# Kernel tuning notes

Measured on AMD Instinct MI355X. Metric: run time of the kernel, lower is better.

The kernel has to match this reference:

```python
import jax, jax.numpy as jnp
import numpy as np


def setup_inputs() -> dict:
    key = jax.random.key(0)
    k1, k2, k3 = jax.random.split(key, 3)
    N, K, H, W = 8, 8, 256, 256
    C, P = 32, 100000
    fragments = jax.random.randint(k1, (N, K, H, W), 0, P, dtype=jnp.int64)
    alphas = jax.random.uniform(k2, (N, K, H, W), dtype=jnp.float32)
    features = jax.random.normal(k3, (C, P), dtype=jnp.float32)
    return {"fragments": fragments, "alphas": alphas, "features": features}


def reference(fragments, alphas, features):
    # Alpha compositing (front-to-back over the K points-per-pixel axis):
    #   weight_k = alpha_k * prod_{j<k} (1 - alpha_j)
    #   out[n,c,h,w] = sum_k weight_k[n,k,h,w] * features[c, fragments[n,k,h,w]]
    # Indices < 0 mark empty fragment slots (sorted to the tail by the
    # rasterizer); treat them as alpha = 0 so they contribute nothing and
    # do not attenuate.
    valid = fragments >= 0                                   # (N,K,H,W)
    a = jnp.where(valid, alphas, 0.0)                        # (N,K,H,W)
    # exclusive cumulative product of transmittance (1 - alpha) along K
    trans = jnp.cumprod(1.0 - a, axis=1)                     # inclusive
    excl = jnp.concatenate(
        [jnp.ones_like(trans[:, :1]), trans[:, :-1]], axis=1
    )                                                        # exclusive
    weights = a * excl                                       # (N,K,H,W)
    idx = jnp.where(valid, fragments, 0)
    gathered = features[:, idx]                              # (C,N,K,H,W)
    images = jnp.einsum("cnkhw,nkhw->nchw", gathered, weights)
    return images
```

## Files before the change

kernel.cpp:

```cpp
#include <hip/hip_runtime.h>
#include <hip/hip_fp16.h>

#define N_IMG 8
#define K_LAY 8
#define C_CH  32
#define P_FEAT 100000
#define HW 65536
#define NPIX (N_IMG * HW)

#define T_EPS 3e-3f

__global__ __launch_bounds__(256) void transpose_feat_h(
    const float* __restrict__ feat, __half* __restrict__ featT)
{
    __shared__ float tile[32][33];
    const int x  = threadIdx.x;
    const int y  = threadIdx.y;
    const int p0 = blockIdx.x * 32;

    #pragma unroll
    for (int j = 0; j < 4; ++j) {
        const int c = y * 4 + j;
        tile[c][x] = feat[(size_t)c * P_FEAT + p0 + x];
    }
    __syncthreads();

    const int t  = x + 32 * y;
    const int pl = t >> 3;
    const int c0 = (t & 7) * 4;
    union { __half h[4]; unsigned long long u; } pk;
    #pragma unroll
    for (int j = 0; j < 4; ++j)
        pk.h[j] = __float2half(tile[c0 + j][pl]);
    *reinterpret_cast<unsigned long long*>(
        featT + (size_t)(p0 + pl) * C_CH + c0) = pk.u;
}

__global__ __launch_bounds__(256) void composite(
    const int*    __restrict__ frag,
    const float*  __restrict__ alpha,
    const __half* __restrict__ featT,
    float*        __restrict__ out)
{
    const int tid = blockIdx.x * 256 + threadIdx.x;
    const int pix = tid >> 2;
    const int q   = tid & 3;
    const int n   = pix >> 16;
    const int p   = pix & (HW - 1);

    const int*   fb = frag  + (size_t)n * K_LAY * HW + p;
    const float* ab = alpha + (size_t)n * K_LAY * HW + p;

    int   f[K_LAY];
    float a[K_LAY];
    #pragma unroll
    for (int k = 0; k < K_LAY; ++k) f[k] = fb[(size_t)k * HW];
    #pragma unroll
    for (int k = 0; k < K_LAY; ++k) a[k] = ab[(size_t)k * HW];

    float w[K_LAY];
    int   idx[K_LAY];
    float T = 1.0f;
    #pragma unroll
    for (int k = 0; k < K_LAY; ++k) {
        const bool  valid = (f[k] >= 0);
        const float ak    = valid ? a[k] : 0.0f;
        const bool  live  = (T >= T_EPS) && valid;
        w[k]   = live ? ak * T : 0.0f;
        idx[k] = live ? f[k] : 0;
        T *= (1.0f - ak);
    }

    float acc[8];
    #pragma unroll
    for (int c = 0; c < 8; ++c) acc[c] = 0.0f;

    #pragma unroll
    for (int k = 0; k < K_LAY; ++k) {
        const float4 r = *reinterpret_cast<const float4*>(
            featT + (size_t)idx[k] * C_CH + q * 8);
        const float wk = w[k];
        const __half2* hp = reinterpret_cast<const __half2*>(&r);
        #pragma unroll
        for (int j = 0; j < 4; ++j) {
            const float2 fj = __half22float2(hp[j]);
            acc[j*2 + 0] = fmaf(wk, fj.x, acc[j*2 + 0]);
            acc[j*2 + 1] = fmaf(wk, fj.y, acc[j*2 + 1]);
        }
    }

    float* ob = out + ((size_t)n * C_CH + q * 8) * HW + p;
    #pragma unroll
    for (int j = 0; j < 8; ++j)
        ob[(size_t)j * HW] = acc[j];
}

__global__ __launch_bounds__(256) void composite_strided(
    const int*   __restrict__ frag,
    const float* __restrict__ alpha,
    const float* __restrict__ feat,
    float*       __restrict__ out)
{
    const int gid = blockIdx.x * 256 + threadIdx.x;
    const int n = gid >> 16;
    const int p = gid & (HW - 1);

    const int*   fb = frag  + (size_t)n * K_LAY * HW + p;
    const float* ab = alpha + (size_t)n * K_LAY * HW + p;

    float acc[C_CH];
    #pragma unroll
    for (int c = 0; c < C_CH; ++c) acc[c] = 0.0f;

    float T = 1.0f;
    #pragma unroll
    for (int k = 0; k < K_LAY; ++k) {
        if (T >= T_EPS) {
            const int   f = fb[(size_t)k * HW];
            float       a = ab[(size_t)k * HW];
            a = (f >= 0) ? a : 0.0f;
            const float wgt = a * T;
            T *= (1.0f - a);
            if (wgt > 0.0f) {
                #pragma unroll
                for (int c = 0; c < C_CH; ++c)
                    acc[c] = fmaf(wgt, feat[(size_t)c * P_FEAT + f], acc[c]);
            }
        }
    }

    float* ob = out + (size_t)n * C_CH * HW + p;
    #pragma unroll
    for (int c = 0; c < C_CH; ++c)
        ob[(size_t)c * HW] = acc[c];
}

extern "C" void kernel_launch(void* const* d_in, const int* in_sizes, int n_in,
                              void* d_out, int out_size, void* d_ws, size_t ws_size,
                              hipStream_t stream)
{
    const int*   frag  = (const int*)  d_in[0];
    const float* alpha = (const float*)d_in[1];
    const float* feat  = (const float*)d_in[2];
    float*       out   = (float*)d_out;

    const size_t need = (size_t)P_FEAT * C_CH * sizeof(__half);
    if (ws_size >= need) {
        __half* featT = (__half*)d_ws;
        transpose_feat_h<<<dim3(P_FEAT / 32), dim3(32, 8), 0, stream>>>(feat, featT);
        composite<<<dim3((NPIX * 4) / 256), dim3(256), 0, stream>>>(frag, alpha, featT, out);
    } else {
        composite_strided<<<dim3(NPIX / 256), dim3(256), 0, stream>>>(frag, alpha, feat, out);
    }
}
```

Baseline: 135.8 us.

## Split fp16 feature table into channel halves mapped to separate XCD groups

The transposed fp16 feature table is split into two channel halves of 16 channels each. Blocks are remapped so that the XCDs in one group of four (by blockIdx modulo 8) each gather only one half, which halves the working set each XCD's L2 has to hold. Fragment and alpha loads and output stores become nontemporal so this streaming data does not evict feature lines from cache. The trade-off is that each pixel's fragments and alphas are now read by two blocks on different XCDs, and the speedup depends on the hardware dispatching blocks round-robin across XCDs.

```diff
diff --git a/kernel.cpp b/kernel.cpp
--- a/kernel.cpp
+++ b/kernel.cpp
@@ -11,7 +11,7 @@
 #define T_EPS 3e-3f
 
 __global__ __launch_bounds__(256) void transpose_feat_h(
-    const float* __restrict__ feat, __half* __restrict__ featT)
+    const float* __restrict__ feat, __half* __restrict__ featH)
 {
     __shared__ float tile[32][33];
     const int x  = threadIdx.x;
@@ -28,25 +28,30 @@
     const int t  = x + 32 * y;
     const int pl = t >> 3;
     const int c0 = (t & 7) * 4;
+    const int half = c0 >> 4;
+    const int cc   = c0 & 15;
     union { __half h[4]; unsigned long long u; } pk;
     #pragma unroll
     for (int j = 0; j < 4; ++j)
         pk.h[j] = __float2half(tile[c0 + j][pl]);
     *reinterpret_cast<unsigned long long*>(
-        featT + (size_t)(p0 + pl) * C_CH + c0) = pk.u;
+        featH + (size_t)half * P_FEAT * 16 + (size_t)(p0 + pl) * 16 + cc) = pk.u;
 }
 
-__global__ __launch_bounds__(256) void composite(
+__global__ __launch_bounds__(256) void composite_split(
     const int*    __restrict__ frag,
     const float*  __restrict__ alpha,
-    const __half* __restrict__ featT,
+    const __half* __restrict__ featH,
     float*        __restrict__ out)
 {
-    const int tid = blockIdx.x * 256 + threadIdx.x;
-    const int pix = tid >> 2;
-    const int q   = tid & 3;
-    const int n   = pix >> 16;
-    const int p   = pix & (HW - 1);
+    const int b    = blockIdx.x;
+    const int xcd  = b & 7;
+    const int half = xcd >> 2;
+    const int pb   = (b >> 3) * 4 + (xcd & 3);
+    const int pix  = pb * 128 + (threadIdx.x >> 1);
+    const int q2   = threadIdx.x & 1;
+    const int n    = pix >> 16;
+    const int p    = pix & (HW - 1);
 
     const int*   fb = frag  + (size_t)n * K_LAY * HW + p;
     const float* ab = alpha + (size_t)n * K_LAY * HW + p;
@@ -54,9 +59,11 @@
     int   f[K_LAY];
     float a[K_LAY];
     #pragma unroll
-    for (int k = 0; k < K_LAY; ++k) f[k] = fb[(size_t)k * HW];
+    for (int k = 0; k < K_LAY; ++k)
+        f[k] = __builtin_nontemporal_load(fb + (size_t)k * HW);
     #pragma unroll
-    for (int k = 0; k < K_LAY; ++k) a[k] = ab[(size_t)k * HW];
+    for (int k = 0; k < K_LAY; ++k)
+        a[k] = __builtin_nontemporal_load(ab + (size_t)k * HW);
 
     float w[K_LAY];
     int   idx[K_LAY];
@@ -75,10 +82,11 @@
     #pragma unroll
     for (int c = 0; c < 8; ++c) acc[c] = 0.0f;
 
+    const __half* tb = featH + (size_t)half * P_FEAT * 16 + q2 * 8;
     #pragma unroll
     for (int k = 0; k < K_LAY; ++k) {
         const float4 r = *reinterpret_cast<const float4*>(
-            featT + (size_t)idx[k] * C_CH + q * 8);
+            tb + (size_t)idx[k] * 16);
         const float wk = w[k];
         const __half2* hp = reinterpret_cast<const __half2*>(&r);
         #pragma unroll
@@ -89,10 +97,10 @@
         }
     }
 
-    float* ob = out + ((size_t)n * C_CH + q * 8) * HW + p;
+    float* ob = out + ((size_t)n * C_CH + half * 16 + q2 * 8) * HW + p;
     #pragma unroll
     for (int j = 0; j < 8; ++j)
-        ob[(size_t)j * HW] = acc[j];
+        __builtin_nontemporal_store(acc[j], ob + (size_t)j * HW);
 }
 
 __global__ __launch_bounds__(256) void composite_strided(
@@ -146,9 +154,10 @@
 
     const size_t need = (size_t)P_FEAT * C_CH * sizeof(__half);
     if (ws_size >= need) {
-        __half* featT = (__half*)d_ws;
-        transpose_feat_h<<<dim3(P_FEAT / 32), dim3(32, 8), 0, stream>>>(feat, featT);
-        composite<<<dim3((NPIX * 4) / 256), dim3(256), 0, stream>>>(frag, alpha, featT, out);
+        __half* featH = (__half*)d_ws;
+        transpose_feat_h<<<dim3(P_FEAT / 32), dim3(32, 8), 0, stream>>>(feat, featH);
+        composite_split<<<dim3((NPIX * 4) / 256), dim3(256), 0, stream>>>(
+            frag, alpha, featH, out);
     } else {
         composite_strided<<<dim3(NPIX / 256), dim3(256), 0, stream>>>(frag, alpha, feat, out);
     }
```

Measured after the change: 147.3 us. +8.5%, slower.
